# Kernel optimization log

Measured on AMD Instinct MI355X. Metric: run time of the kernel, lower is better.

The kernel has to match this reference:

```python
import jax, jax.numpy as jnp
import numpy as np

B, N, D = 8, 2048, 1024

def setup_inputs() -> dict:
    key = jax.random.key(0)
    k1, k2, k3, k4 = jax.random.split(key, 4)
    q = jax.random.normal(k1, (B, N, D), dtype=jnp.float32)
    k = jax.random.normal(k2, (B, N, D), dtype=jnp.float32)
    v = jax.random.uniform(k3, (B, N, N), dtype=jnp.float32)
    # nn.Linear default init (kaiming-uniform-ish); scale is irrelevant for correctness
    bound = 1.0 / np.sqrt(D)
    W1 = jax.random.uniform(k4, (D, D), dtype=jnp.float32, minval=-bound, maxval=bound)
    b1 = jnp.zeros((D,), dtype=jnp.float32)
    return {"q": q, "k": k, "v": v, "W1": W1, "b1": b1}

def adj_normalization(adj):
    # D^{-1/2} A D^{-1/2} with rowsum clamped at 1; expressed as O(N^2)
    # broadcast scaling instead of the original's two diagonal bmms.
    rowsum = jnp.maximum(adj.sum(-1), 1.0)          # [B, N]
    d_inv_sqrt = rowsum ** -0.5                      # [B, N]
    return d_inv_sqrt[:, :, None] * adj * d_inv_sqrt[:, None, :]

def reference(q, k, v, W1, b1):
    # ff_layers == 1: q_out = linear1(q) (dropout is identity in eval);
    # k is unused because _fc returns (q_out, q_out).
    q_out = jnp.einsum('bnd,ed->bne', q, W1) + b1    # [B, N, D]
    attn = jnp.einsum('bnd,bmd->bnm', q_out, q_out)  # [B, N, N]
    # comb_mode == 2 (learn_n_norm): symmetric normalization of attn; v unused.
    output = adj_normalization(attn)
    return (output, attn)
```

## Files before the change

kernel.cpp:

```cpp
#include <hip/hip_runtime.h>

#define B_ 8
#define N_ 2048
#define D_ 1024

using u16 = unsigned short;
typedef __attribute__((ext_vector_type(8))) short short8;
typedef __attribute__((ext_vector_type(4))) float f32x4;
typedef __attribute__((ext_vector_type(4))) float float4v;
typedef __attribute__((ext_vector_type(4))) int int4v;

static __device__ __forceinline__ float bf2f(u16 h) {
  return __uint_as_float(((unsigned)h) << 16);
}
static __device__ __forceinline__ u16 f2bf(float f) {
  unsigned u = __float_as_uint(f);
  u += 0x7FFFu + ((u >> 16) & 1u);
  return (u16)(u >> 16);
}

static __device__ __forceinline__ void gload16(const void* g, void* l) {
  __builtin_amdgcn_global_load_lds((const __attribute__((address_space(1))) void*)g,
                                   (__attribute__((address_space(3))) void*)l, 16, 0, 0);
}

static __device__ __forceinline__ void stage_slab(u16* __restrict__ L,
                                                  const u16* __restrict__ g,
                                                  int slab, int kof, int w) {
  gload16(g + (size_t)(slab * 64) * 1024 + kof, L + slab * 4096 + w * 512);
}


template<int S1, int S2, int VM>
__device__ __forceinline__ void tile_body(u16* __restrict__ cur, u16* __restrict__ nxt,
                                          const u16* __restrict__ gA, const u16* __restrict__ gB,
                                          int kn1, int kn2,
                                          int w, int wr, int wc, int lane15, int ck0,
                                          f32x4 (&acc)[8][4])
{
  const u16* Ar = cur + (wr * 128 + lane15) * 64;
  const u16* Br = cur + 16384 + (wc * 64 + lane15) * 64;
  const int ck1 = ck0 ^ 32;
  short8 a[4], bk0[4], bk1[4];

  if constexpr (VM == 2) asm volatile("s_waitcnt vmcnt(2)" ::: "memory");
  else                   asm volatile("s_waitcnt vmcnt(0)" ::: "memory");
  __builtin_amdgcn_s_barrier();

  #pragma unroll
  for (int m = 0; m < 4; ++m) a[m] = *(const short8*)(Ar + m * 1024 + ck0);
  #pragma unroll
  for (int n = 0; n < 4; ++n) bk0[n] = *(const short8*)(Br + n * 1024 + ck0);
  if constexpr (S1) { stage_slab(nxt, gA, 1, kn1, w); stage_slab(nxt, gA, 3, kn1, w); }
  __builtin_amdgcn_s_barrier();
  __builtin_amdgcn_s_setprio(1);
  #pragma unroll
  for (int m = 0; m < 4; ++m)
    #pragma unroll
    for (int n = 0; n < 4; ++n)
      acc[m][n] = __builtin_amdgcn_mfma_f32_16x16x32_bf16(a[m], bk0[n], acc[m][n], 0, 0, 0);
  __builtin_amdgcn_s_setprio(0);
  __builtin_amdgcn_s_barrier();

  #pragma unroll
  for (int m = 0; m < 4; ++m) a[m] = *(const short8*)(Ar + m * 1024 + ck1);
  #pragma unroll
  for (int n = 0; n < 4; ++n) bk1[n] = *(const short8*)(Br + n * 1024 + ck1);
  if constexpr (S1) { stage_slab(nxt + 16384, gB, 0, kn1, w); stage_slab(nxt + 16384, gB, 1, kn1, w); }
  __builtin_amdgcn_s_barrier();
  __builtin_amdgcn_s_setprio(1);
  #pragma unroll
  for (int m = 0; m < 4; ++m)
    #pragma unroll
    for (int n = 0; n < 4; ++n)
      acc[m][n] = __builtin_amdgcn_mfma_f32_16x16x32_bf16(a[m], bk1[n], acc[m][n], 0, 0, 0);
  __builtin_amdgcn_s_setprio(0);
  __builtin_amdgcn_s_barrier();

  #pragma unroll
  for (int m = 0; m < 4; ++m) a[m] = *(const short8*)(Ar + (m + 4) * 1024 + ck0);
  if constexpr (S1) { stage_slab(nxt + 16384, gB, 2, kn1, w); stage_slab(nxt + 16384, gB, 3, kn1, w); }
  __builtin_amdgcn_s_barrier();
  __builtin_amdgcn_s_setprio(1);
  #pragma unroll
  for (int m = 0; m < 4; ++m)
    #pragma unroll
    for (int n = 0; n < 4; ++n)
      acc[m + 4][n] = __builtin_amdgcn_mfma_f32_16x16x32_bf16(a[m], bk0[n], acc[m + 4][n], 0, 0, 0);
  __builtin_amdgcn_s_setprio(0);
  __builtin_amdgcn_s_barrier();

  #pragma unroll
  for (int m = 0; m < 4; ++m) a[m] = *(const short8*)(Ar + (m + 4) * 1024 + ck1);
  if constexpr (S2) { stage_slab(cur, gA, 0, kn2, w); stage_slab(cur, gA, 2, kn2, w); }
  __builtin_amdgcn_s_barrier();
  __builtin_amdgcn_s_setprio(1);
  #pragma unroll
  for (int m = 0; m < 4; ++m)
    #pragma unroll
    for (int n = 0; n < 4; ++n)
      acc[m + 4][n] = __builtin_amdgcn_mfma_f32_16x16x32_bf16(a[m], bk1[n], acc[m + 4][n], 0, 0, 0);
  __builtin_amdgcn_s_setprio(0);
  __builtin_amdgcn_s_barrier();
}

template<int MODE>
__global__ __launch_bounds__(512, 2)
void gemm8p(const u16* __restrict__ Abase, const u16* __restrict__ Bbase,
            const float* __restrict__ aux,
            void* __restrict__ C0, float* __restrict__ C1)
{
  __shared__ u16 lds[2][32768];
  const int tid = threadIdx.x;
  const int w = tid >> 6, l = tid & 63;

  int tm0, tn0, z = 0;
  if (MODE == 0) {
    const int bid = blockIdx.x;
    const int s = (bid & 7) * 32 + (bid >> 3);
    tm0 = (s >> 2) << 8;
    tn0 = (s & 3) << 8;
  } else {
    const int bid = blockIdx.x;
    const int s = (bid & 7) * 64 + (bid >> 3);
    z  = s >> 6;
    tm0 = ((s >> 3) & 7) << 8;
    tn0 = (s & 7) << 8;
  }
  const u16* A  = Abase + (MODE ? (size_t)z * N_ * D_ : 0);
  const u16* Bm = (MODE ? A : Bbase);

  const int sc = (((l & 7) ^ (l >> 3)) << 4) >> 1;
  const int sr = w * 8 + (l >> 3);
  const u16* gA = A  + (size_t)(tm0 + sr) * 1024 + sc;
  const u16* gB = Bm + (size_t)(tn0 + sr) * 1024 + sc;

  const int lane15 = l & 15, lhi = l >> 4;
  const int ck0 = ((lhi << 4) ^ ((l & 7) << 4)) >> 1;
  const int wr = w >> 2, wc = w & 3;

  f32x4 acc[8][4];
  #pragma unroll
  for (int m = 0; m < 8; ++m)
    #pragma unroll
    for (int n = 0; n < 4; ++n)
      acc[m][n] = (f32x4){0.f, 0.f, 0.f, 0.f};

  u16* cur = &lds[0][0];
  u16* nxt = &lds[1][0];

  #pragma unroll
  for (int s4 = 0; s4 < 4; ++s4) stage_slab(cur, gA, s4, 0, w);
  #pragma unroll
  for (int s4 = 0; s4 < 4; ++s4) stage_slab(cur + 16384, gB, s4, 0, w);
  stage_slab(nxt, gA, 0, 64, w);
  stage_slab(nxt, gA, 2, 64, w);

  for (int t = 0; t < 14; ++t) {
    tile_body<1, 1, 2>(cur, nxt, gA, gB, (t + 1) * 64, (t + 2) * 64,
                       w, wr, wc, lane15, ck0, acc);
    u16* tmp = cur; cur = nxt; nxt = tmp;
  }
  tile_body<1, 0, 2>(cur, nxt, gA, gB, 15 * 64, 0, w, wr, wc, lane15, ck0, acc);
  { u16* tmp = cur; cur = nxt; nxt = tmp; }
  tile_body<0, 0, 0>(cur, nxt, gA, gB, 0, 0, w, wr, wc, lane15, ck0, acc);
  asm volatile("s_waitcnt vmcnt(0)" ::: "memory");

  const int rbase = tm0 + wr * 128 + lhi * 4;
  const int cbase = tn0 + wc * 64 + lane15;

  if (MODE == 0) {
    u16* C = (u16*)C0;
    #pragma unroll
    for (int m = 0; m < 8; ++m)
      #pragma unroll
      for (int n = 0; n < 4; ++n) {
        const int col = cbase + n * 16;
        const float bv = aux[col];
        #pragma unroll
        for (int j = 0; j < 4; ++j)
          C[(size_t)(rbase + m * 16 + j) * 1024 + col] = f2bf(acc[m][n][j] + bv);
      }
  } else {
    float* Cattn = (float*)C0 + (size_t)z * N_ * N_;
    float* Cout  = C1 + (size_t)z * N_ * N_;
    const float* dv = aux + z * N_;
    float di[8][4];
    #pragma unroll
    for (int m = 0; m < 8; ++m)
      #pragma unroll
      for (int j = 0; j < 4; ++j)
        di[m][j] = dv[rbase + m * 16 + j];
    #pragma unroll
    for (int m = 0; m < 8; ++m)
      #pragma unroll
      for (int n = 0; n < 4; ++n) {
        const int col = cbase + n * 16;
        const float dj = dv[col];
        #pragma unroll
        for (int j = 0; j < 4; ++j) {
          const size_t off = (size_t)(rbase + m * 16 + j) * N_ + col;
          const float a = acc[m][n][j];
          Cattn[off] = a;
          Cout[off]  = a * di[m][j] * dj;
        }
      }
  }
}

__global__ void cvt_q_qsum(const float* __restrict__ q, u16* __restrict__ qbf,
                           float* __restrict__ qsum) {
  const int wi = blockIdx.x * 256 + threadIdx.x;
  const int d0 = (wi & 127) * 8;
  const int rc = (wi >> 7) & 127;
  const int b  = wi >> 14;
  const size_t base = ((size_t)b * N_ + rc * 16) * D_ + d0;
  float s[8];
  #pragma unroll
  for (int k = 0; k < 8; ++k) s[k] = 0.f;
  #pragma unroll 4
  for (int r = 0; r < 16; ++r) {
    const float4v* p = (const float4v*)(q + base + (size_t)r * D_);
    float4v x = p[0], y = p[1];
    union { u16 h[8]; int4v v; } o;
    o.h[0] = f2bf(x.x); o.h[1] = f2bf(x.y); o.h[2] = f2bf(x.z); o.h[3] = f2bf(x.w);
    o.h[4] = f2bf(y.x); o.h[5] = f2bf(y.y); o.h[6] = f2bf(y.z); o.h[7] = f2bf(y.w);
    *(int4v*)(qbf + base + (size_t)r * D_) = o.v;
    s[0] += x.x; s[1] += x.y; s[2] += x.z; s[3] += x.w;
    s[4] += y.x; s[5] += y.y; s[6] += y.z; s[7] += y.w;
  }
  float* qs = qsum + b * D_ + d0;
  #pragma unroll
  for (int k = 0; k < 8; ++k) atomicAdd(qs + k, s[k]);
}

__global__ void cvt_f32_to_bf16(const float* __restrict__ in, u16* __restrict__ out, int n8) {
  const int stride = gridDim.x * blockDim.x;
  for (int i = blockIdx.x * blockDim.x + threadIdx.x; i < n8; i += stride) {
    const float4v* p = (const float4v*)in + (size_t)i * 2;
    float4v a = p[0], b = p[1];
    union { u16 h[8]; int4v v; } r;
    r.h[0] = f2bf(a.x); r.h[1] = f2bf(a.y); r.h[2] = f2bf(a.z); r.h[3] = f2bf(a.w);
    r.h[4] = f2bf(b.x); r.h[5] = f2bf(b.y); r.h[6] = f2bf(b.z); r.h[7] = f2bf(b.w);
    ((int4v*)out)[i] = r.v;
  }
}

__global__ void s_kernel(const float* __restrict__ qsum, const float* __restrict__ W1,
                         const float* __restrict__ b1, float* __restrict__ s) {
  const int idx = blockIdx.x * 256 + threadIdx.x;
  const int b = idx >> 10, e = idx & (D_ - 1);
  const int d0 = blockIdx.y * 64;
  const float4v* wp = (const float4v*)(W1 + (size_t)e * D_ + d0);
  const float4v* qp = (const float4v*)(qsum + b * D_ + d0);
  float acc = 0.f;
  #pragma unroll 4
  for (int t = 0; t < 16; ++t) {
    float4v wv = wp[t], qv = qp[t];
    acc += wv.x * qv.x + wv.y * qv.y + wv.z * qv.z + wv.w * qv.w;
  }
  if (blockIdx.y == 0) acc += (float)N_ * b1[e];
  atomicAdd(&s[b * D_ + e], acc);
}

__global__ void t_kernel(const float* __restrict__ W1, const float* __restrict__ s,
                         float* __restrict__ tv) {
  const int idx = blockIdx.x * 256 + threadIdx.x;
  const int b = idx >> 10, d = idx & (D_ - 1);
  const int e0 = blockIdx.y * 64;
  const float* wp = W1 + (size_t)e0 * D_ + d;
  const float* sp = s + b * D_ + e0;
  float acc = 0.f;
  #pragma unroll 8
  for (int e = 0; e < 64; ++e) acc += wp[(size_t)e * D_] * sp[e];
  atomicAdd(&tv[b * D_ + d], acc);
}

__global__ void c_kernel(const float* __restrict__ b1, const float* __restrict__ s,
                         float* __restrict__ c) {
  const int b = blockIdx.x;
  const int tid = threadIdx.x;
  float acc = 0.f;
  #pragma unroll
  for (int t = 0; t < 4; ++t) {
    const int e = tid + t * 256;
    acc += b1[e] * s[b * D_ + e];
  }
  __shared__ float red[4];
  #pragma unroll
  for (int off = 32; off; off >>= 1) acc += __shfl_down(acc, off);
  if ((tid & 63) == 0) red[tid >> 6] = acc;
  __syncthreads();
  if (tid == 0) c[b] = red[0] + red[1] + red[2] + red[3];
}

__global__ void rowdinv_kernel(const float* __restrict__ q, const float* __restrict__ tv,
                               const float* __restrict__ c, float* __restrict__ dinv) {
  const int row  = blockIdx.x * 4 + (threadIdx.x >> 6);
  const int lane = threadIdx.x & 63;
  const int b    = row >> 11;
  const float4v* p  = (const float4v*)(q + (size_t)row * D_);
  const float4v* tp = (const float4v*)(tv + b * D_);
  float acc = 0.f;
  #pragma unroll
  for (int it = 0; it < 4; ++it) {
    float4v qv = p[it * 64 + lane];
    float4v tw = tp[it * 64 + lane];
    acc += qv.x * tw.x + qv.y * tw.y + qv.z * tw.z + qv.w * tw.w;
  }
  #pragma unroll
  for (int off = 32; off; off >>= 1) acc += __shfl_down(acc, off);
  if (lane == 0) dinv[row] = rsqrtf(fmaxf(acc + c[b], 1.0f));
}

extern "C" void kernel_launch(void* const* d_in, const int* in_sizes, int n_in,
                              void* d_out, int out_size, void* d_ws, size_t ws_size,
                              hipStream_t stream) {
  const float* q  = (const float*)d_in[0];
  const float* W1 = (const float*)d_in[3];
  const float* b1 = (const float*)d_in[4];

  float* out  = (float*)d_out;
  float* attn = out + (size_t)B_ * N_ * N_;

  char* ws = (char*)d_ws;
  u16*   qbf  = (u16*)ws;
  u16*   qout = (u16*)(ws + (size_t)33554432);
  u16*   w1bf = (u16*)(ws + (size_t)67108864);
  float* qsum = (float*)(ws + (size_t)69206016);
  float* s    = (float*)(ws + (size_t)69238784);
  float* tv   = (float*)(ws + (size_t)69271552);
  float* c    = (float*)(ws + (size_t)69304320);
  float* dinv = (float*)(ws + (size_t)69304576);

  hipMemsetAsync(qsum, 0, 3 * B_ * D_ * sizeof(float) + 256, stream);

  cvt_q_qsum<<<512, 256, 0, stream>>>(q, qbf, qsum);
  cvt_f32_to_bf16<<<512, 256, 0, stream>>>(W1, w1bf, D_ * D_ / 8);

  gemm8p<0><<<256, 512, 0, stream>>>(qbf, w1bf, b1, qout, nullptr);

  s_kernel<<<dim3(B_ * D_ / 256, 16), 256, 0, stream>>>(qsum, W1, b1, s);
  t_kernel<<<dim3(B_ * D_ / 256, 16), 256, 0, stream>>>(W1, s, tv);
  c_kernel<<<B_, 256, 0, stream>>>(b1, s, c);
  rowdinv_kernel<<<(B_ * N_) / 4, 256, 0, stream>>>(q, tv, c, dinv);

  gemm8p<1><<<512, 512, 0, stream>>>(qout, nullptr, dinv, attn, out);
}
```

Baseline: 217.1 us.

## Exploit Gram symmetry: compute upper-triangular tiles and mirror via LDS transpose

```diff
diff --git a/kernel.cpp b/kernel.cpp
--- a/kernel.cpp
+++ b/kernel.cpp
@@ -122,10 +122,13 @@
     tn0 = (s & 3) << 8;
   } else {
     const int bid = blockIdx.x;
-    const int s = (bid & 7) * 64 + (bid >> 3);
-    z  = s >> 6;
-    tm0 = ((s >> 3) & 7) << 8;
-    tn0 = (s & 7) << 8;
+    z = bid & 7;
+    int rem = bid >> 3;
+    int i = 0;
+    while (rem >= 8 - i) { rem -= 8 - i; ++i; }
+    const int j = i + rem;
+    tm0 = i << 8;
+    tn0 = j << 8;
   }
   const u16* A  = Abase + (MODE ? (size_t)z * N_ * D_ : 0);
   const u16* Bm = (MODE ? A : Bbase);
@@ -185,6 +188,7 @@
     float* Cattn = (float*)C0 + (size_t)z * N_ * N_;
     float* Cout  = C1 + (size_t)z * N_ * N_;
     const float* dv = aux + z * N_;
+
     float di[8][4];
     #pragma unroll
     for (int m = 0; m < 8; ++m)
@@ -205,44 +209,79 @@
           Cout[off]  = a * di[m][j] * dj;
         }
       }
-  }
-}
-
-__global__ void cvt_q_qsum(const float* __restrict__ q, u16* __restrict__ qbf,
-                           float* __restrict__ qsum) {
-  const int wi = blockIdx.x * 256 + threadIdx.x;
-  const int d0 = (wi & 127) * 8;
-  const int rc = (wi >> 7) & 127;
-  const int b  = wi >> 14;
-  const size_t base = ((size_t)b * N_ + rc * 16) * D_ + d0;
-  float s[8];
-  #pragma unroll
-  for (int k = 0; k < 8; ++k) s[k] = 0.f;
-  #pragma unroll 4
-  for (int r = 0; r < 16; ++r) {
-    const float4v* p = (const float4v*)(q + base + (size_t)r * D_);
-    float4v x = p[0], y = p[1];
-    union { u16 h[8]; int4v v; } o;
-    o.h[0] = f2bf(x.x); o.h[1] = f2bf(x.y); o.h[2] = f2bf(x.z); o.h[3] = f2bf(x.w);
-    o.h[4] = f2bf(y.x); o.h[5] = f2bf(y.y); o.h[6] = f2bf(y.z); o.h[7] = f2bf(y.w);
-    *(int4v*)(qbf + base + (size_t)r * D_) = o.v;
-    s[0] += x.x; s[1] += x.y; s[2] += x.z; s[3] += x.w;
-    s[4] += y.x; s[5] += y.y; s[6] += y.z; s[7] += y.w;
-  }
-  float* qs = qsum + b * D_ + d0;
-  #pragma unroll
-  for (int k = 0; k < 8; ++k) atomicAdd(qs + k, s[k]);
-}
-
-__global__ void cvt_f32_to_bf16(const float* __restrict__ in, u16* __restrict__ out, int n8) {
-  const int stride = gridDim.x * blockDim.x;
-  for (int i = blockIdx.x * blockDim.x + threadIdx.x; i < n8; i += stride) {
-    const float4v* p = (const float4v*)in + (size_t)i * 2;
+
+    if (tm0 != tn0) {
+      float* trb = (float*)(&lds[0][0]) + w * (32 * 68);
+      #pragma unroll
+      for (int h = 0; h < 2; ++h) {
+        const int colg0 = tm0 + wr * 128 + h * 64;
+        const float4v dj4 = *(const float4v*)(dv + colg0 + lane15 * 4);
+        #pragma unroll
+        for (int p = 0; p < 2; ++p) {
+          #pragma unroll
+          for (int mm = 0; mm < 4; ++mm)
+            #pragma unroll
+            for (int np = 0; np < 2; ++np)
+              #pragma unroll
+              for (int j = 0; j < 4; ++j)
+                trb[(np * 16 + lane15) * 68 + lhi * 4 + mm * 16 + j] =
+                    acc[h * 4 + mm][2 * p + np][j];
+          const int rowg0 = tn0 + wc * 64 + p * 32;
+          #pragma unroll
+          for (int it = 0; it < 8; ++it) {
+            const int cc = it * 4 + lhi;
+            const float4v vv = *(const float4v*)(trb + cc * 68 + lane15 * 4);
+            const int rg = rowg0 + cc;
+            const float dic = dv[rg];
+            const size_t off = (size_t)rg * N_ + colg0 + lane15 * 4;
+            *(float4v*)(Cattn + off) = vv;
+            float4v ov;
+            ov.x = vv.x * dic * dj4.x;
+            ov.y = vv.y * dic * dj4.y;
+            ov.z = vv.z * dic * dj4.z;
+            ov.w = vv.w * dic * dj4.w;
+            *(float4v*)(Cout + off) = ov;
+          }
+        }
+      }
+    }
+  }
+}
+
+__global__ void cvt_fused(const float* __restrict__ q, u16* __restrict__ qbf,
+                          float* __restrict__ qsum,
+                          const float* __restrict__ W1, u16* __restrict__ w1bf) {
+  if (blockIdx.x < 512) {
+    const int wi = blockIdx.x * 256 + threadIdx.x;
+    const int d0 = (wi & 127) * 8;
+    const int rc = (wi >> 7) & 127;
+    const int b  = wi >> 14;
+    const size_t base = ((size_t)b * N_ + rc * 16) * D_ + d0;
+    float s[8];
+    #pragma unroll
+    for (int k = 0; k < 8; ++k) s[k] = 0.f;
+    #pragma unroll 4
+    for (int r = 0; r < 16; ++r) {
+      const float4v* p = (const float4v*)(q + base + (size_t)r * D_);
+      float4v x = p[0], y = p[1];
+      union { u16 h[8]; int4v v; } o;
+      o.h[0] = f2bf(x.x); o.h[1] = f2bf(x.y); o.h[2] = f2bf(x.z); o.h[3] = f2bf(x.w);
+      o.h[4] = f2bf(y.x); o.h[5] = f2bf(y.y); o.h[6] = f2bf(y.z); o.h[7] = f2bf(y.w);
+      *(int4v*)(qbf + base + (size_t)r * D_) = o.v;
+      s[0] += x.x; s[1] += x.y; s[2] += x.z; s[3] += x.w;
+      s[4] += y.x; s[5] += y.y; s[6] += y.z; s[7] += y.w;
+    }
+    float* qs = qsum + b * D_ + d0;
+    #pragma unroll
+    for (int k = 0; k < 8; ++k) atomicAdd(qs + k, s[k]);
+  } else {
+    const int i = (blockIdx.x - 512) * 256 + threadIdx.x;
+    const float4v* p = (const float4v*)W1 + (size_t)i * 2;
     float4v a = p[0], b = p[1];
     union { u16 h[8]; int4v v; } r;
     r.h[0] = f2bf(a.x); r.h[1] = f2bf(a.y); r.h[2] = f2bf(a.z); r.h[3] = f2bf(a.w);
     r.h[4] = f2bf(b.x); r.h[5] = f2bf(b.y); r.h[6] = f2bf(b.z); r.h[7] = f2bf(b.w);
-    ((int4v*)out)[i] = r.v;
+    ((int4v*)w1bf)[i] = r.v;
   }
 }
 
@@ -263,35 +302,35 @@
   atomicAdd(&s[b * D_ + e], acc);
 }
 
-__global__ void t_kernel(const float* __restrict__ W1, const float* __restrict__ s,
-                         float* __restrict__ tv) {
-  const int idx = blockIdx.x * 256 + threadIdx.x;
-  const int b = idx >> 10, d = idx & (D_ - 1);
-  const int e0 = blockIdx.y * 64;
-  const float* wp = W1 + (size_t)e0 * D_ + d;
-  const float* sp = s + b * D_ + e0;
-  float acc = 0.f;
-  #pragma unroll 8
-  for (int e = 0; e < 64; ++e) acc += wp[(size_t)e * D_] * sp[e];
-  atomicAdd(&tv[b * D_ + d], acc);
-}
-
-__global__ void c_kernel(const float* __restrict__ b1, const float* __restrict__ s,
-                         float* __restrict__ c) {
-  const int b = blockIdx.x;
-  const int tid = threadIdx.x;
-  float acc = 0.f;
-  #pragma unroll
-  for (int t = 0; t < 4; ++t) {
-    const int e = tid + t * 256;
-    acc += b1[e] * s[b * D_ + e];
-  }
-  __shared__ float red[4];
-  #pragma unroll
-  for (int off = 32; off; off >>= 1) acc += __shfl_down(acc, off);
-  if ((tid & 63) == 0) red[tid >> 6] = acc;
-  __syncthreads();
-  if (tid == 0) c[b] = red[0] + red[1] + red[2] + red[3];
+__global__ void tc_kernel(const float* __restrict__ W1, const float* __restrict__ s,
+                          const float* __restrict__ b1,
+                          float* __restrict__ tv, float* __restrict__ c) {
+  if (blockIdx.y < 16) {
+    const int idx = blockIdx.x * 256 + threadIdx.x;
+    const int b = idx >> 10, d = idx & (D_ - 1);
+    const int e0 = blockIdx.y * 64;
+    const float* wp = W1 + (size_t)e0 * D_ + d;
+    const float* sp = s + b * D_ + e0;
+    float acc = 0.f;
+    #pragma unroll 8
+    for (int e = 0; e < 64; ++e) acc += wp[(size_t)e * D_] * sp[e];
+    atomicAdd(&tv[b * D_ + d], acc);
+  } else if (blockIdx.x < 8) {
+    const int b = blockIdx.x;
+    const int tid = threadIdx.x;
+    float acc = 0.f;
+    #pragma unroll
+    for (int t = 0; t < 4; ++t) {
+      const int e = tid + t * 256;
+      acc += b1[e] * s[b * D_ + e];
+    }
+    __shared__ float red[4];
+    #pragma unroll
+    for (int off = 32; off; off >>= 1) acc += __shfl_down(acc, off);
+    if ((tid & 63) == 0) red[tid >> 6] = acc;
+    __syncthreads();
+    if (tid == 0) c[b] = red[0] + red[1] + red[2] + red[3];
+  }
 }
 
 __global__ void rowdinv_kernel(const float* __restrict__ q, const float* __restrict__ tv,
@@ -335,15 +374,13 @@
 
   hipMemsetAsync(qsum, 0, 3 * B_ * D_ * sizeof(float) + 256, stream);
 
-  cvt_q_qsum<<<512, 256, 0, stream>>>(q, qbf, qsum);
-  cvt_f32_to_bf16<<<512, 256, 0, stream>>>(W1, w1bf, D_ * D_ / 8);
+  cvt_fused<<<1024, 256, 0, stream>>>(q, qbf, qsum, W1, w1bf);
 
   gemm8p<0><<<256, 512, 0, stream>>>(qbf, w1bf, b1, qout, nullptr);
 
   s_kernel<<<dim3(B_ * D_ / 256, 16), 256, 0, stream>>>(qsum, W1, b1, s);
-  t_kernel<<<dim3(B_ * D_ / 256, 16), 256, 0, stream>>>(W1, s, tv);
-  c_kernel<<<B_, 256, 0, stream>>>(b1, s, c);
+  tc_kernel<<<dim3(B_ * D_ / 256, 17), 256, 0, stream>>>(W1, s, b1, tv, c);
   rowdinv_kernel<<<(B_ * N_) / 4, 256, 0, stream>>>(q, tv, c, dinv);
 
-  gemm8p<1><<<512, 512, 0, stream>>>(qout, nullptr, dinv, attn, out);
-}
+  gemm8p<1><<<288, 512, 0, stream>>>(qout, nullptr, dinv, attn, out);
+}
```

Measured after the change: 228.9 us. 5.4% more time.
